# Kernel tuning notes

Hardware: AMD Instinct MI355X
Metric: run time of the kernel (lower is better)

The kernel has to match this reference:

```python
import jax, jax.numpy as jnp
import numpy as np


def _make_dplr(N):
    # HiPPO-NPLR -> diagonalized (p, q, lambda), matching _make_p_q_lambda
    idx = np.arange(1, N + 1)
    hippo = np.where(
        idx[:, None] > idx[None, :],
        np.sqrt(2.0 * idx[:, None] + 1.0) * np.sqrt(2.0 * idx[None, :] + 1.0),
        np.where(idx[:, None] == idx[None, :], idx[:, None] + 1.0, 0.0),
    )
    p = 0.5 * np.sqrt(2.0 * idx + 1.0)
    q = 2.0 * p
    S = -hippo + p[:, None] * q[None, :]
    lam, V = np.linalg.eig(S)
    Vc = V.conj().T
    return Vc @ p.astype(np.complex128), Vc @ q.conj().astype(np.complex128), lam


def _ri(x):
    # complex -> [..., 2] float32 (torch.view_as_real layout)
    return np.stack([x.real, x.imag], axis=-1).astype(np.float32)


def setup_inputs() -> dict:
    D_MODEL, N, L_MAX, BATCH = 512, 64, 2048, 16
    key = jax.random.key(0)
    k_u, k_B, k_Ct, k_step = jax.random.split(key, 4)
    p, q, lam = _make_dplr(N)
    std = float(np.sqrt(2.0 / (D_MODEL + N)))  # xavier_normal gain=1
    B_ri = jax.random.normal(k_B, (D_MODEL, N, 2), dtype=jnp.float32) * (std / np.sqrt(2.0))
    Ct_ri = jax.random.normal(k_Ct, (D_MODEL, N, 2), dtype=jnp.float32) * (std / np.sqrt(2.0))
    dt_min, dt_max = 1e-3, 1e-1
    log_step = (jax.random.uniform(k_step, (D_MODEL,), dtype=jnp.float32)
                * float(np.log(dt_max) - np.log(dt_min)) + float(np.log(dt_min)))
    u = jax.random.normal(k_u, (BATCH, L_MAX, D_MODEL), dtype=jnp.float32)
    return {
        'u': u,
        'p_ri': jnp.asarray(_ri(p)),
        'q_ri': jnp.asarray(_ri(q)),
        'lam_ri': jnp.asarray(_ri(lam)),
        'B_ri': B_ri,
        'Ct_ri': Ct_ri,
        'D': jnp.ones((1, 1, D_MODEL), jnp.float32),
        'log_step': log_step,
    }


def _to_c(x):
    return jax.lax.complex(x[..., 0], x[..., 1])


def reference(u, p_ri, q_ri, lam_ri, B_ri, Ct_ri, D, log_step):
    l_max = u.shape[1]
    p, q, lam = _to_c(p_ri), _to_c(q_ri), _to_c(lam_ri)
    B, Ct = _to_c(B_ri), _to_c(Ct_ri)
    # roots of unity omega_l
    omega = jnp.exp((2j * np.pi / l_max) * jnp.arange(l_max)).astype(jnp.complex64)
    step = jnp.exp(log_step)
    g = jnp.outer(2.0 / step, (1.0 - omega) / (1.0 + omega))   # [d, L] complex
    c = 2.0 / (1.0 + omega)                                    # [L]
    # fused Cauchy kernel: one reciprocal tensor shared by all four dots
    r = 1.0 / (g[:, :, None] - lam[None, None, :])             # [d, L, n]
    a0, a1, b0, b1 = Ct.conj(), q.conj(), B, p
    k00 = jnp.einsum('dn,dln->dl', a0 * b0, r)
    k01 = jnp.einsum('dn,dln->dl', a0 * b1, r)
    k10 = jnp.einsum('dn,dln->dl', a1 * b0, r)
    k11 = jnp.einsum('n,dln->dl', a1 * b1, r)
    at_roots = c * (k00 - k01 * k10 / (1.0 + k11))             # [d, L]
    out = jnp.fft.ifft(at_roots, n=l_max, axis=-1)
    # ifft reordering: [0, L-1, L-2, ..., 1]
    order = jnp.concatenate([jnp.zeros((1,), jnp.int32), jnp.arange(l_max - 1, 0, -1, dtype=jnp.int32)])
    K = out[:, order].real[None]                               # [1, d, L]
    # non-circular (linear) convolution via length-2L FFT
    ud = jnp.fft.rfft(jnp.pad(u, ((0, 0), (0, l_max), (0, 0))), axis=1)   # [B, L+1, d]
    Kd = jnp.fft.rfft(jnp.pad(K, ((0, 0), (0, 0), (0, l_max))), axis=-1)  # [1, d, L+1]
    y = jnp.fft.irfft(jnp.swapaxes(ud, -2, -1) * Kd, axis=-1)[..., :l_max]
    return jnp.swapaxes(y, -2, -1) + D * u
```

## Files before the change

### kernel.cpp

```cpp
#include <hip/hip_runtime.h>

#define LMAX   2048
#define NFFT   4096
#define DMODEL 512
#define NSTATE 64
#define NBATCH 16
#define PI_D   3.14159265358979323846
#define REC_STRIDE 2050

#define PAD(e) ((e) + ((e) >> 4))


__device__ __forceinline__ float2 cmul(float2 a, float2 b) {
  return make_float2(a.x*b.x - a.y*b.y, a.x*b.y + a.y*b.x);
}
__device__ __forceinline__ float rcpf(float x) { return __builtin_amdgcn_rcpf(x); }

template<bool INV>
__device__ __forceinline__ void bf8(float2 x[8]) {
  const float r2 = 0.70710678118654752f;
  float2 E0,E1,E2,E3,O0,O1,O2,O3;
  {
    float2 u0 = make_float2(x[0].x+x[4].x, x[0].y+x[4].y);
    float2 v0 = make_float2(x[0].x-x[4].x, x[0].y-x[4].y);
    float2 u1 = make_float2(x[2].x+x[6].x, x[2].y+x[6].y);
    float2 v1 = make_float2(x[2].x-x[6].x, x[2].y-x[6].y);
    E0 = make_float2(u0.x+u1.x, u0.y+u1.y);
    E2 = make_float2(u0.x-u1.x, u0.y-u1.y);
    if (!INV) { E1 = make_float2(v0.x+v1.y, v0.y-v1.x); E3 = make_float2(v0.x-v1.y, v0.y+v1.x); }
    else      { E1 = make_float2(v0.x-v1.y, v0.y+v1.x); E3 = make_float2(v0.x+v1.y, v0.y-v1.x); }
  }
  {
    float2 u0 = make_float2(x[1].x+x[5].x, x[1].y+x[5].y);
    float2 v0 = make_float2(x[1].x-x[5].x, x[1].y-x[5].y);
    float2 u1 = make_float2(x[3].x+x[7].x, x[3].y+x[7].y);
    float2 v1 = make_float2(x[3].x-x[7].x, x[3].y-x[7].y);
    O0 = make_float2(u0.x+u1.x, u0.y+u1.y);
    O2 = make_float2(u0.x-u1.x, u0.y-u1.y);
    if (!INV) { O1 = make_float2(v0.x+v1.y, v0.y-v1.x); O3 = make_float2(v0.x-v1.y, v0.y+v1.x); }
    else      { O1 = make_float2(v0.x-v1.y, v0.y+v1.x); O3 = make_float2(v0.x+v1.y, v0.y-v1.x); }
  }
  float2 o1 = (!INV) ? make_float2((O1.x+O1.y)*r2, (O1.y-O1.x)*r2)
                     : make_float2((O1.x-O1.y)*r2, (O1.y+O1.x)*r2);
  float2 o2 = (!INV) ? make_float2(O2.y, -O2.x) : make_float2(-O2.y, O2.x);
  float2 o3 = (!INV) ? make_float2((O3.y-O3.x)*r2, -(O3.x+O3.y)*r2)
                     : make_float2(-(O3.x+O3.y)*r2, (O3.x-O3.y)*r2);
  x[0] = make_float2(E0.x+O0.x, E0.y+O0.y);
  x[4] = make_float2(E0.x-O0.x, E0.y-O0.y);
  x[1] = make_float2(E1.x+o1.x, E1.y+o1.y);
  x[5] = make_float2(E1.x-o1.x, E1.y-o1.y);
  x[2] = make_float2(E2.x+o2.x, E2.y+o2.y);
  x[6] = make_float2(E2.x-o2.x, E2.y-o2.y);
  x[3] = make_float2(E3.x+o3.x, E3.y+o3.y);
  x[7] = make_float2(E3.x-o3.x, E3.y-o3.y);
}

__device__ __forceinline__ void bf4(float2 x[4]) {
  float2 u0 = make_float2(x[0].x+x[2].x, x[0].y+x[2].y);
  float2 v0 = make_float2(x[0].x-x[2].x, x[0].y-x[2].y);
  float2 u1 = make_float2(x[1].x+x[3].x, x[1].y+x[3].y);
  float2 v1 = make_float2(x[1].x-x[3].x, x[1].y-x[3].y);
  x[0] = make_float2(u0.x+u1.x, u0.y+u1.y);
  x[2] = make_float2(u0.x-u1.x, u0.y-u1.y);
  x[1] = make_float2(v0.x+v1.y, v0.y-v1.x);
  x[3] = make_float2(v0.x-v1.y, v0.y+v1.x);
}

template<int LOGN, bool INV, int NT>
__device__ float2* fft_lds(float2* src, float2* dst, const float2* __restrict__ tw, int tid) {
  constexpr int N = 1 << LOGN;
  constexpr int NS8 = LOGN / 3;
  constexpr int TSH = 12 - LOGN;
  int s = 1;
  #pragma unroll
  for (int st = 0; st < NS8; ++st) {
    __syncthreads();
    for (int i = tid; i < (N >> 3); i += NT) {
      const int q  = i & (s - 1);
      const int ps = i - q;
      float2 x[8];
      #pragma unroll
      for (int k = 0; k < 8; ++k) x[k] = src[PAD(i + k * (N >> 3))];
      bf8<INV>(x);
      const int idx1 = ps << TSH;
      const int ob   = q + (ps << 3);
      dst[PAD(ob)] = x[0];
      #pragma unroll
      for (int j = 1; j < 8; ++j) {
        float2 w = tw[j * idx1];
        if (INV) w.y = -w.y;
        dst[PAD(ob + j * s)] = cmul(w, x[j]);
      }
    }
    s <<= 3;
    float2* t = src; src = dst; dst = t;
  }
  if constexpr (LOGN % 3 == 2) {
    __syncthreads();
    for (int i = tid; i < (N >> 2); i += NT) {
      const int q  = i & (s - 1);
      const int ps = i - q;
      float2 x[4];
      #pragma unroll
      for (int k = 0; k < 4; ++k) x[k] = src[PAD(i + k * (N >> 2))];
      bf4(x);
      const int ob = q + (ps << 2);
      #pragma unroll
      for (int j = 0; j < 4; ++j) dst[PAD(ob + j * s)] = x[j];
    }
    float2* t = src; src = dst; dst = t;
  }
  __syncthreads();
  return src;
}

__global__ void twiddle_init(float2* tw) {
  int j = blockIdx.x * blockDim.x + threadIdx.x;
  if (j < NFFT) {
    double ang = -2.0 * PI_D * (double)j / (double)NFFT;
    double s, c;
    sincos(ang, &s, &c);
    tw[j] = make_float2((float)c, (float)s);
  }
}

__global__ __launch_bounds__(256) void s4_cauchy(
    const float* __restrict__ p_ri, const float* __restrict__ q_ri,
    const float* __restrict__ lam_ri, const float* __restrict__ B_ri,
    const float* __restrict__ Ct_ri, const float* __restrict__ log_step,
    float2* __restrict__ atr)
{
  __shared__ float2 Wg[5*64];
  const int d = blockIdx.x;
  const int tid = threadIdx.x;
  const int l = blockIdx.y * 256 + tid;

  if (tid < NSTATE) {
    const int n = tid;
    float2 la = make_float2(lam_ri[2*n], lam_ri[2*n+1]);
    float2 pp = make_float2(p_ri[2*n],  p_ri[2*n+1]);
    float2 qq = make_float2(q_ri[2*n],  q_ri[2*n+1]);
    float2 Bv = make_float2(B_ri[(d*NSTATE+n)*2],  B_ri[(d*NSTATE+n)*2+1]);
    float2 Cv = make_float2(Ct_ri[(d*NSTATE+n)*2], Ct_ri[(d*NSTATE+n)*2+1]);
    Wg[n] = la;
    Wg[64 +n] = make_float2(Cv.x*Bv.x + Cv.y*Bv.y, Cv.x*Bv.y - Cv.y*Bv.x);
    Wg[128+n] = make_float2(Cv.x*pp.x + Cv.y*pp.y, Cv.x*pp.y - Cv.y*pp.x);
    Wg[192+n] = make_float2(qq.x*Bv.x + qq.y*Bv.y, qq.x*Bv.y - qq.y*Bv.x);
    Wg[256+n] = make_float2(qq.x*pp.x + qq.y*pp.y, qq.x*pp.y - qq.y*pp.x);
  }
  __syncthreads();

  const float tos = 2.0f * rcpf(expf(log_step[d]));
  float theta = (float)(2.0 * PI_D / (double)LMAX) * (float)l;
  float si, co;
  sincosf(theta, &si, &co);
  float dx = 1.f + co, dy = si;
  float inv = rcpf(dx*dx + dy*dy);
  float2 cc = make_float2(2.f*dx*inv, -2.f*dy*inv);
  float nx = 1.f - co, ny = -si;
  float2 g = make_float2(tos*(nx*dx + ny*dy)*inv, tos*(ny*dx - nx*dy)*inv);

  float2 a00 = {0,0}, a01 = {0,0}, a10 = {0,0}, a11 = {0,0};
  for (int nc = 0; nc < NSTATE; nc += 4) {
    float2 la[4], w0[4], w1[4], w2[4], w3[4];
    #pragma unroll
    for (int j=0;j<4;j++) {
      la[j] = Wg[nc+j];      w0[j] = Wg[64+nc+j];  w1[j] = Wg[128+nc+j];
      w2[j] = Wg[192+nc+j];  w3[j] = Wg[256+nc+j];
    }
    #pragma unroll
    for (int j=0;j<4;j++) {
      float rr = g.x - la[j].x, ri = g.y - la[j].y;
      float rinv = rcpf(rr*rr + ri*ri);
      float rx = rr*rinv, ry = -ri*rinv;
      a00.x += w0[j].x*rx - w0[j].y*ry; a00.y += w0[j].x*ry + w0[j].y*rx;
      a01.x += w1[j].x*rx - w1[j].y*ry; a01.y += w1[j].x*ry + w1[j].y*rx;
      a10.x += w2[j].x*rx - w2[j].y*ry; a10.y += w2[j].x*ry + w2[j].y*rx;
      a11.x += w3[j].x*rx - w3[j].y*ry; a11.y += w3[j].x*ry + w3[j].y*rx;
    }
  }
  float2 s1 = make_float2(1.f + a11.x, a11.y);
  float sinv = rcpf(s1.x*s1.x + s1.y*s1.y);
  float2 t = cmul(a01, a10);
  float2 tdiv = make_float2((t.x*s1.x + t.y*s1.y)*sinv, (t.y*s1.x - t.x*s1.y)*sinv);
  atr[(size_t)d * LMAX + l] = cmul(cc, make_float2(a00.x - tdiv.x, a00.y - tdiv.y));
}

__global__ __launch_bounds__(256) void s4_fftK(
    const float2* __restrict__ atr, const float2* __restrict__ tw,
    float* __restrict__ Ktime)
{
  __shared__ float2 ZA[PAD(LMAX-1)+2], ZB[PAD(LMAX-1)+2];
  const int d = blockIdx.x;
  const int tid = threadIdx.x;
  const float2* src = atr + (size_t)d * LMAX;
  #pragma unroll
  for (int k=0; k<8; ++k) { const int l = tid + (k<<8); ZA[PAD(l)] = src[l]; }
  float2* Z = fft_lds<11, false, 256>(ZA, ZB, tw, tid);
  #pragma unroll
  for (int k=0; k<8; ++k) {
    const int kk = tid + (k<<8);
    Ktime[(size_t)d * LMAX + kk] = Z[PAD(kk)].x * (1.0f / LMAX);
  }
}

__global__ __launch_bounds__(512) void s4_pairB(
    const float* __restrict__ Ktime, const float2* __restrict__ tw,
    float4* __restrict__ Kd)
{
  __shared__ float2 ZA[PAD(NFFT-1)+2], ZB[PAD(NFFT-1)+2];
  const int dp = blockIdx.x;
  const int tid = threadIdx.x;
  const float* K0p = Ktime + (size_t)(2*dp) * LMAX;
  const float* K1p = K0p + LMAX;
  #pragma unroll
  for (int il=0; il<4; ++il) {
    const int kk = tid + (il<<9);
    ZA[PAD(kk)] = make_float2(K0p[kk], K1p[kk]);
    ZA[PAD(LMAX + kk)] = make_float2(0.f, 0.f);
  }
  float2* Z = fft_lds<12, false, 512>(ZA, ZB, tw, tid);
  float4* rec = Kd + (size_t)dp * REC_STRIDE;
  #pragma unroll
  for (int it=0; it<5; ++it) {
    int t = tid + (it<<9);
    if (it == 4) { if (tid != 0) break; t = 2048; }
    float2 zf = Z[PAD(t)];
    float2 zr = Z[PAD((NFFT - t) & (NFFT-1))];
    float k0x = 0.5f*(zf.x + zr.x), k0y = 0.5f*(zf.y - zr.y);
    float dx = zf.x - zr.x, dy = zf.y + zr.y;
    rec[t] = make_float4(k0x, k0y, 0.5f*dy, -0.5f*dx);
  }
}

__global__ __launch_bounds__(512) void s4_conv(
    const float* __restrict__ u, const float* __restrict__ Dp,
    const float2* __restrict__ tw, const float4* __restrict__ Kd,
    float* __restrict__ out)
{
  __shared__ float2 ZA[PAD(NFFT-1)+2], ZB[PAD(NFFT-1)+2];
  const int bxr = blockIdx.x;
  const int dp  = (bxr & 7) * 32 + (bxr >> 3);
  const int b   = blockIdx.y;
  const int d0  = dp * 2;
  const int tid = threadIdx.x;

  float2 ur[4];
  const float* ubase = u + ((size_t)b * LMAX) * DMODEL + d0;
  #pragma unroll
  for (int k=0; k<4; ++k) {
    const int l = tid + (k<<9);
    float2 v = *(const float2*)(ubase + (size_t)l * DMODEL);
    ur[k] = v;
    ZA[PAD(l)] = v;
    ZA[PAD(LMAX + l)] = make_float2(0.f, 0.f);
  }

  float2* Z = fft_lds<12, false, 512>(ZA, ZB, tw, tid);

  const float4* rec = Kd + (size_t)dp * REC_STRIDE;
  #pragma unroll
  for (int it=0; it<5; ++it) {
    int t = tid + (it<<9);
    if (it == 4) { if (tid != 0) break; t = 2048; }
    const int j1 = PAD(t);
    const int j2 = PAD((NFFT - t) & (NFFT-1));
    float2 zf = Z[j1], zr = Z[j2];
    float4 r4 = rec[t];
    float2 K0 = make_float2(r4.x, r4.y), K1 = make_float2(r4.z, r4.w);
    float2 u0 = make_float2(0.5f*(zf.x + zr.x), 0.5f*(zf.y - zr.y));
    float du_x = zf.x - zr.x, du_y = zf.y + zr.y;
    float2 u1 = make_float2(0.5f*du_y, -0.5f*du_x);
    float2 P = cmul(u0, K0);
    float2 Q = cmul(u1, K1);
    Z[j1] = make_float2(P.x - Q.y, P.y + Q.x);
    Z[j2] = make_float2(P.x + Q.y, Q.x - P.y);
  }

  float2* W = fft_lds<12, true, 512>(Z, (Z == ZA) ? ZB : ZA, tw, tid);

  const float D0 = Dp[d0], D1 = Dp[d0 + 1];
  float* obase = out + ((size_t)b * LMAX) * DMODEL + d0;
  const float scale = 1.0f / NFFT;
  #pragma unroll
  for (int k=0; k<4; ++k) {
    const int l = tid + (k<<9);
    float2 w = W[PAD(l)];
    float2 o = make_float2(w.x*scale + D0*ur[k].x, w.y*scale + D1*ur[k].y);
    *(float2*)(obase + (size_t)l * DMODEL) = o;
  }
}

extern "C" void kernel_launch(void* const* d_in, const int* in_sizes, int n_in,
                              void* d_out, int out_size, void* d_ws, size_t ws_size,
                              hipStream_t stream) {
  const float* u        = (const float*)d_in[0];
  const float* p_ri     = (const float*)d_in[1];
  const float* q_ri     = (const float*)d_in[2];
  const float* lam_ri   = (const float*)d_in[3];
  const float* B_ri     = (const float*)d_in[4];
  const float* Ct_ri    = (const float*)d_in[5];
  const float* Dp       = (const float*)d_in[6];
  const float* log_step = (const float*)d_in[7];
  float* out = (float*)d_out;

  char* wsb = (char*)d_ws;
  float2* tw    = (float2*)wsb;
  float4* Kd    = (float4*)(wsb + NFFT * sizeof(float2));
  float2* atr   = (float2*)Kd;
  float*  Ktime = (float*)(wsb + NFFT * sizeof(float2)
                               + (size_t)256 * REC_STRIDE * sizeof(float4));

  twiddle_init<<<16, 256, 0, stream>>>(tw);
  s4_cauchy<<<dim3(DMODEL, 8), 256, 0, stream>>>(p_ri, q_ri, lam_ri, B_ri, Ct_ri,
                                                 log_step, atr);
  s4_fftK<<<DMODEL, 256, 0, stream>>>(atr, tw, Ktime);
  s4_pairB<<<DMODEL/2, 512, 0, stream>>>(Ktime, tw, Kd);
  s4_conv<<<dim3(DMODEL/2, NBATCH), 512, 0, stream>>>(u, Dp, tw, Kd, out);
}
```

Before: 332.3 us.

## Restructure conv FFT in-place with register radix-8 stages; batch Cauchy over four l

The convolution kernel now runs its 4096-point forward and inverse FFTs as four radix-8 stages with a single LDS buffer. The first forward stage is done in registers straight from the loaded input, exploiting the zero-padded upper half, and the last inverse stage feeds the output store directly. This halves LDS use so more blocks can be resident, and cuts LDS round trips, at the cost of an extra barrier per stage. The Cauchy kernel now computes four sequence positions per thread, reusing each shared-memory weight load across them with a quarter of the blocks. A dead index term in the radix-4 tail is also dropped.

New measurement: 509.5 us. +53.4%, slower.

```diff
diff --git a/kernel.cpp b/kernel.cpp
--- a/kernel.cpp
+++ b/kernel.cpp
@@ -99,12 +99,11 @@
     __syncthreads();
     for (int i = tid; i < (N >> 2); i += NT) {
       const int q  = i & (s - 1);
-      const int ps = i - q;
       float2 x[4];
       #pragma unroll
       for (int k = 0; k < 4; ++k) x[k] = src[PAD(i + k * (N >> 2))];
       bf4(x);
-      const int ob = q + (ps << 2);
+      const int ob = q;
       #pragma unroll
       for (int j = 0; j < 4; ++j) dst[PAD(ob + j * s)] = x[j];
     }
@@ -112,6 +111,26 @@
   }
   __syncthreads();
   return src;
+}
+
+template<bool INV, int S>
+__device__ __forceinline__ void conv_stage(float2* Z, const float2* __restrict__ tw, int tid) {
+  float2 x[8];
+  #pragma unroll
+  for (int k = 0; k < 8; ++k) x[k] = Z[PAD(tid + (k << 9))];
+  __syncthreads();
+  bf8<INV>(x);
+  const int q  = tid & (S - 1);
+  const int ps = tid - q;
+  const int ob = q + (ps << 3);
+  Z[PAD(ob)] = x[0];
+  #pragma unroll
+  for (int j = 1; j < 8; ++j) {
+    float2 w = tw[j * ps];
+    if (INV) w.y = -w.y;
+    Z[PAD(ob + j * S)] = cmul(w, x[j]);
+  }
+  __syncthreads();
 }
 
 __global__ void twiddle_init(float2* tw) {
@@ -124,7 +143,7 @@
   }
 }
 
-__global__ __launch_bounds__(256) void s4_cauchy(
+__global__ __launch_bounds__(256, 4) void s4_cauchy(
     const float* __restrict__ p_ri, const float* __restrict__ q_ri,
     const float* __restrict__ lam_ri, const float* __restrict__ B_ri,
     const float* __restrict__ Ct_ri, const float* __restrict__ log_step,
@@ -133,7 +152,7 @@
   __shared__ float2 Wg[5*64];
   const int d = blockIdx.x;
   const int tid = threadIdx.x;
-  const int l = blockIdx.y * 256 + tid;
+  const int l0 = blockIdx.y * 1024;
 
   if (tid < NSTATE) {
     const int n = tid;
@@ -151,39 +170,56 @@
   __syncthreads();
 
   const float tos = 2.0f * rcpf(expf(log_step[d]));
-  float theta = (float)(2.0 * PI_D / (double)LMAX) * (float)l;
-  float si, co;
-  sincosf(theta, &si, &co);
-  float dx = 1.f + co, dy = si;
-  float inv = rcpf(dx*dx + dy*dy);
-  float2 cc = make_float2(2.f*dx*inv, -2.f*dy*inv);
-  float nx = 1.f - co, ny = -si;
-  float2 g = make_float2(tos*(nx*dx + ny*dy)*inv, tos*(ny*dx - nx*dy)*inv);
-
-  float2 a00 = {0,0}, a01 = {0,0}, a10 = {0,0}, a11 = {0,0};
-  for (int nc = 0; nc < NSTATE; nc += 4) {
-    float2 la[4], w0[4], w1[4], w2[4], w3[4];
+  float2 g[4], cc[4];
+  #pragma unroll
+  for (int il = 0; il < 4; ++il) {
+    const int l = l0 + (il << 8) + tid;
+    float theta = (float)(2.0 * PI_D / (double)LMAX) * (float)l;
+    float si, co;
+    sincosf(theta, &si, &co);
+    float dx = 1.f + co, dy = si;
+    float inv = rcpf(dx*dx + dy*dy);
+    cc[il] = make_float2(2.f*dx*inv, -2.f*dy*inv);
+    float nx = 1.f - co, ny = -si;
+    g[il] = make_float2(tos*(nx*dx + ny*dy)*inv, tos*(ny*dx - nx*dy)*inv);
+  }
+
+  float2 a00[4], a01[4], a10[4], a11[4];
+  #pragma unroll
+  for (int il = 0; il < 4; ++il) {
+    a00[il] = make_float2(0,0); a01[il] = make_float2(0,0);
+    a10[il] = make_float2(0,0); a11[il] = make_float2(0,0);
+  }
+  for (int nc = 0; nc < NSTATE; nc += 2) {
+    float2 la[2], w0[2], w1[2], w2[2], w3[2];
     #pragma unroll
-    for (int j=0;j<4;j++) {
+    for (int j = 0; j < 2; ++j) {
       la[j] = Wg[nc+j];      w0[j] = Wg[64+nc+j];  w1[j] = Wg[128+nc+j];
       w2[j] = Wg[192+nc+j];  w3[j] = Wg[256+nc+j];
     }
     #pragma unroll
-    for (int j=0;j<4;j++) {
-      float rr = g.x - la[j].x, ri = g.y - la[j].y;
-      float rinv = rcpf(rr*rr + ri*ri);
-      float rx = rr*rinv, ry = -ri*rinv;
-      a00.x += w0[j].x*rx - w0[j].y*ry; a00.y += w0[j].x*ry + w0[j].y*rx;
-      a01.x += w1[j].x*rx - w1[j].y*ry; a01.y += w1[j].x*ry + w1[j].y*rx;
-      a10.x += w2[j].x*rx - w2[j].y*ry; a10.y += w2[j].x*ry + w2[j].y*rx;
-      a11.x += w3[j].x*rx - w3[j].y*ry; a11.y += w3[j].x*ry + w3[j].y*rx;
+    for (int il = 0; il < 4; ++il) {
+      #pragma unroll
+      for (int j = 0; j < 2; ++j) {
+        float rr = g[il].x - la[j].x, ri = g[il].y - la[j].y;
+        float rinv = rcpf(rr*rr + ri*ri);
+        float rx = rr*rinv, ry = -ri*rinv;
+        a00[il].x += w0[j].x*rx - w0[j].y*ry; a00[il].y += w0[j].x*ry + w0[j].y*rx;
+        a01[il].x += w1[j].x*rx - w1[j].y*ry; a01[il].y += w1[j].x*ry + w1[j].y*rx;
+        a10[il].x += w2[j].x*rx - w2[j].y*ry; a10[il].y += w2[j].x*ry + w2[j].y*rx;
+        a11[il].x += w3[j].x*rx - w3[j].y*ry; a11[il].y += w3[j].x*ry + w3[j].y*rx;
+      }
     }
   }
-  float2 s1 = make_float2(1.f + a11.x, a11.y);
-  float sinv = rcpf(s1.x*s1.x + s1.y*s1.y);
-  float2 t = cmul(a01, a10);
-  float2 tdiv = make_float2((t.x*s1.x + t.y*s1.y)*sinv, (t.y*s1.x - t.x*s1.y)*sinv);
-  atr[(size_t)d * LMAX + l] = cmul(cc, make_float2(a00.x - tdiv.x, a00.y - tdiv.y));
+  #pragma unroll
+  for (int il = 0; il < 4; ++il) {
+    const int l = l0 + (il << 8) + tid;
+    float2 s1 = make_float2(1.f + a11[il].x, a11[il].y);
+    float sinv = rcpf(s1.x*s1.x + s1.y*s1.y);
+    float2 t = cmul(a01[il], a10[il]);
+    float2 tdiv = make_float2((t.x*s1.x + t.y*s1.y)*sinv, (t.y*s1.x - t.x*s1.y)*sinv);
+    atr[(size_t)d * LMAX + l] = cmul(cc[il], make_float2(a00[il].x - tdiv.x, a00[il].y - tdiv.y));
+  }
 }
 
 __global__ __launch_bounds__(256) void s4_fftK(
@@ -233,12 +269,12 @@
   }
 }
 
-__global__ __launch_bounds__(512) void s4_conv(
+__global__ __launch_bounds__(512, 8) void s4_conv(
     const float* __restrict__ u, const float* __restrict__ Dp,
     const float2* __restrict__ tw, const float4* __restrict__ Kd,
     float* __restrict__ out)
 {
-  __shared__ float2 ZA[PAD(NFFT-1)+2], ZB[PAD(NFFT-1)+2];
+  __shared__ float2 Z[PAD(NFFT-1)+1];
   const int bxr = blockIdx.x;
   const int dp  = (bxr & 7) * 32 + (bxr >> 3);
   const int b   = blockIdx.y;
@@ -246,17 +282,27 @@
   const int tid = threadIdx.x;
 
   float2 ur[4];
+  float2 x[8];
   const float* ubase = u + ((size_t)b * LMAX) * DMODEL + d0;
   #pragma unroll
   for (int k=0; k<4; ++k) {
-    const int l = tid + (k<<9);
-    float2 v = *(const float2*)(ubase + (size_t)l * DMODEL);
-    ur[k] = v;
-    ZA[PAD(l)] = v;
-    ZA[PAD(LMAX + l)] = make_float2(0.f, 0.f);
-  }
-
-  float2* Z = fft_lds<12, false, 512>(ZA, ZB, tw, tid);
+    ur[k] = *(const float2*)(ubase + (size_t)(tid + (k<<9)) * DMODEL);
+    x[k] = ur[k];
+  }
+  #pragma unroll
+  for (int k=4; k<8; ++k) x[k] = make_float2(0.f, 0.f);
+  bf8<false>(x);
+  {
+    const int ob = tid << 3;
+    Z[PAD(ob)] = x[0];
+    #pragma unroll
+    for (int j=1; j<8; ++j) Z[PAD(ob + j)] = cmul(tw[j*tid], x[j]);
+  }
+  __syncthreads();
+
+  conv_stage<false, 8>  (Z, tw, tid);
+  conv_stage<false, 64> (Z, tw, tid);
+  conv_stage<false, 512>(Z, tw, tid);
 
   const float4* rec = Kd + (size_t)dp * REC_STRIDE;
   #pragma unroll
@@ -276,18 +322,22 @@
     Z[j1] = make_float2(P.x - Q.y, P.y + Q.x);
     Z[j2] = make_float2(P.x + Q.y, Q.x - P.y);
   }
-
-  float2* W = fft_lds<12, true, 512>(Z, (Z == ZA) ? ZB : ZA, tw, tid);
-
+  __syncthreads();
+
+  conv_stage<true, 1> (Z, tw, tid);
+  conv_stage<true, 8> (Z, tw, tid);
+  conv_stage<true, 64>(Z, tw, tid);
+
+  #pragma unroll
+  for (int k=0; k<8; ++k) x[k] = Z[PAD(tid + (k<<9))];
+  bf8<true>(x);
   const float D0 = Dp[d0], D1 = Dp[d0 + 1];
   float* obase = out + ((size_t)b * LMAX) * DMODEL + d0;
   const float scale = 1.0f / NFFT;
   #pragma unroll
-  for (int k=0; k<4; ++k) {
-    const int l = tid + (k<<9);
-    float2 w = W[PAD(l)];
-    float2 o = make_float2(w.x*scale + D0*ur[k].x, w.y*scale + D1*ur[k].y);
-    *(float2*)(obase + (size_t)l * DMODEL) = o;
+  for (int j=0; j<4; ++j) {
+    float2 o = make_float2(x[j].x*scale + D0*ur[j].x, x[j].y*scale + D1*ur[j].y);
+    *(float2*)(obase + (size_t)(tid + (j<<9)) * DMODEL) = o;
   }
 }
 
@@ -312,7 +362,7 @@
                                + (size_t)256 * REC_STRIDE * sizeof(float4));
 
   twiddle_init<<<16, 256, 0, stream>>>(tw);
-  s4_cauchy<<<dim3(DMODEL, 8), 256, 0, stream>>>(p_ri, q_ri, lam_ri, B_ri, Ct_ri,
+  s4_cauchy<<<dim3(DMODEL, 2), 256, 0, stream>>>(p_ri, q_ri, lam_ri, B_ri, Ct_ri,
                                                  log_step, atr);
   s4_fftK<<<DMODEL, 256, 0, stream>>>(atr, tw, Ktime);
   s4_pairB<<<DMODEL/2, 512, 0, stream>>>(Ktime, tw, Kd);
```
